# Kernel optimization log

Hardware: AMD Instinct MI355X
Metric: run time of the kernel (lower is better)

Reference implementation:

```python
import jax, jax.numpy as jnp
import numpy as np
from jax import lax

B, S, C = 32, 512, 32          # batch, seq_len (words), char_len
V, E = 101, 64                 # char vocab (printable + pad), emb size
F, K = 128, 3                  # n_filters, kernel_size


def setup_inputs() -> dict:
    key = jax.random.key(0)
    k0, k1, k2, k3 = jax.random.split(key, 4)
    char_ids = jax.random.randint(k0, (B, S, C), 0, V, dtype=jnp.int32)
    emb_table = jax.random.normal(k1, (V, E), dtype=jnp.float32)
    emb_table = emb_table.at[0].set(0.0)  # padding_idx=0
    fan_in = E * K
    conv_w = jax.random.normal(k2, (F, E, K), dtype=jnp.float32) / np.sqrt(fan_in)
    conv_b = jax.random.normal(k3, (F,), dtype=jnp.float32) * 0.01
    return {"char_ids": char_ids, "emb_table": emb_table,
            "conv_w": conv_w, "conv_b": conv_b}


def reference(char_ids, emb_table, conv_w, conv_b):
    b, s, c = char_ids.shape
    e = emb_table.shape[1]
    # embedding lookup: [B, S, C, E]; dropout p=0.0 (eval) -> identity
    char_embs = emb_table[char_ids]
    # FAITHFUL to torch source: .view(-1, E, C) is a raw row-major
    # reinterpretation of the contiguous [B*S, C, E] buffer (not a permute).
    x = char_embs.reshape(b * s, e, c)  # [B*S, E, C] by memory layout
    # Conv1d over the last axis, valid padding
    y = lax.conv_general_dilated(
        x, conv_w, window_strides=(1,), padding="VALID",
        dimension_numbers=("NCH", "OIH", "NCH"))  # [B*S, F, C-K+1]
    y = y + conv_b[None, :, None]
    # max-pool over time, then back to [B, S, F]
    return y.max(axis=2).reshape(b, s, -1)
```

## Files before the change

### kernel.cpp

```cpp
#include <hip/hip_runtime.h>
#include <cstdint>


typedef __bf16 bf16x8 __attribute__((ext_vector_type(8)));
typedef float  f32x16 __attribute__((ext_vector_type(16)));

#define GW   4
#define NGRP 4
#define NW   16
#define ROWS 34
#define RST  72

__global__ __launch_bounds__(256)
void prep_pack_w(const float* __restrict__ w, __bf16* __restrict__ pw) {
  int i = blockIdx.x * 256 + threadIdx.x;
  int j    = i & 7;
  int lane = (i >> 3) & 63;
  int ks   = (i >> 9) & 3;
  int t    = i >> 11;
  int kk   = t % 3;
  int nt   = t / 3;
  int f = nt * 32 + (lane & 31);
  int e = ks * 16 + (lane >> 5) * 8 + j;
  pw[i] = (__bf16)w[f * 192 + e * 3 + kk];
}

__global__ __launch_bounds__(256, 2)
void charcnn_mfma(const int* __restrict__ cid, const float* __restrict__ emb,
                  const float* __restrict__ bias, const __bf16* __restrict__ pw,
                  float* __restrict__ out) {
  __shared__ __align__(16) __bf16 xT[8][ROWS * RST];

  const int tid  = threadIdx.x;
  const int lane = tid & 63;
  const int wv   = tid >> 6;
  const int np   = wv & 1;
  const int ws   = wv >> 1;

  bf16x8 bfrag[2][12];
  const bf16x8* pwv = (const bf16x8*)pw;
#pragma unroll
  for (int nt = 0; nt < 2; ++nt)
#pragma unroll
    for (int q = 0; q < 12; ++q)
      bfrag[nt][q] = pwv[((np * 2 + nt) * 12 + q) * 64 + lane];

  const float vb0 = bias[(np * 2 + 0) * 32 + (lane & 31)];
  const float vb1 = bias[(np * 2 + 1) * 32 + (lane & 31)];

  const int a  = tid >> 3;
  const int p  = tid & 7;
  const int d0 = p * 4;
  const int bw = blockIdx.x * NW;

  int chw[NW];
#pragma unroll
  for (int w = 0; w < NW; ++w) chw[w] = cid[(bw + w) * 32 + a];

  float4 slo[GW], shi[GW];

  auto stage_load = [&](int g) {
#pragma unroll
    for (int i = 0; i < GW; ++i) {
      const float4* er = (const float4*)(emb + chw[g * GW + i] * 64);
      slo[i] = er[p];
      shi[i] = er[p + 8];
    }
  };

  auto stage_write = [&](int g) {
    const int w0 = g * GW;
#pragma unroll
    for (int i = 0; i < GW; ++i) {
      uint32_t* dst = (uint32_t*)(&xT[(w0 + i) & 7][0]);
      float lv[4] = {slo[i].x, slo[i].y, slo[i].z, slo[i].w};
      float hv[4] = {shi[i].x, shi[i].y, shi[i].z, shi[i].w};
#pragma unroll
      for (int i2 = 0; i2 < 4; ++i2) {
        uint32_t u = ((uint32_t)__builtin_bit_cast(uint16_t, (__bf16)hv[i2]) << 16)
                   |  (uint32_t)__builtin_bit_cast(uint16_t, (__bf16)lv[i2]);
        dst[(d0 + i2) * 36 + a] = u;
      }
    }
  };

  auto finish = [&](const f32x16& acc, float vbv, int fcol, int w) {
    float m01 = fmaxf(acc[0],  acc[1]);
    float m23 = fmaxf(acc[2],  acc[3]);
    float m45 = fmaxf(acc[4],  acc[5]);
    float m67 = fmaxf(acc[6],  acc[7]);
    float m89 = fmaxf(acc[8],  acc[9]);
    float mab = fmaxf(acc[10], acc[11]);
    float mcd = fmaxf(acc[12], acc[13]);
    float q0 = fmaxf(m01, m23);
    float q1 = fmaxf(m45, m67);
    float q2 = fmaxf(m89, mab);
    float m0 = fmaxf(fmaxf(q0, q1), fmaxf(q2, mcd));
    float m1 = fmaxf(acc[14], acc[15]);
    float mm = (lane < 32) ? fmaxf(m0, m1) : m0;
    float other = __shfl_xor(mm, 32, 64);
    float fullmax = fmaxf(mm, other) + vbv;
    if (lane < 32) out[(bw + w) * 128 + fcol + lane] = fullmax;
  };

  auto compute_word = [&](int w) {
    const __bf16* xb = &xT[w & 7][0] + (lane & 31) * RST + (lane >> 5) * 8;
    f32x16 acc0, acc1;
#pragma unroll
    for (int r = 0; r < 16; ++r) { acc0[r] = 0.0f; acc1[r] = 0.0f; }

#pragma unroll
    for (int kk = 0; kk < 3; ++kk) {
#pragma unroll
      for (int ks = 0; ks < 4; ++ks) {
        bf16x8 av = *(const bf16x8*)(xb + kk * RST + ks * 16);
        acc0 = __builtin_amdgcn_mfma_f32_32x32x16_bf16(av, bfrag[0][kk * 4 + ks],
                                                       acc0, 0, 0, 0);
        acc1 = __builtin_amdgcn_mfma_f32_32x32x16_bf16(av, bfrag[1][kk * 4 + ks],
                                                       acc1, 0, 0, 0);
      }
    }
    finish(acc0, vb0, np * 64,      w);
    finish(acc1, vb1, np * 64 + 32, w);
  };

  stage_load(0);
  stage_write(0);
  __syncthreads();

#pragma unroll
  for (int g = 0; g < NGRP; ++g) {
    if (g + 1 < NGRP) stage_load(g + 1);
    compute_word(g * GW + ws);
    compute_word(g * GW + ws + 2);
    if (g + 1 < NGRP) stage_write(g + 1);
    if (g + 1 < NGRP) __syncthreads();
  }
}

extern "C" void kernel_launch(void* const* d_in, const int* in_sizes, int n_in,
                              void* d_out, int out_size, void* d_ws, size_t ws_size,
                              hipStream_t stream) {
  const int*   cid = (const int*)d_in[0];
  const float* emb = (const float*)d_in[1];
  const float* cw  = (const float*)d_in[2];
  const float* cb  = (const float*)d_in[3];
  float* outp = (float*)d_out;
  __bf16* pw = (__bf16*)d_ws;

  hipLaunchKernelGGL(prep_pack_w, dim3(96), dim3(256), 0, stream, cw, pw);
  hipLaunchKernelGGL(charcnn_mfma, dim3(1024), dim3(256), 0, stream,
                     cid, emb, cb, (const __bf16*)pw, outp);
}
```

Baseline: 35.10 us.

## Double-buffer embedding prefetch two groups ahead and raise MFMA wave priority

Halves the staging group size to two words and keeps two register buffers of gathered embedding rows. Loads now run two groups ahead, and each group's LDS write happens before the barrier, so the gather latency can hide behind more compute. The plain sync is replaced by an LDS-only waitcnt plus s_barrier, and the MFMA loop is wrapped in s_setprio to favour matrix work. In exchange there are more barriers per block (eight instead of three) and higher register pressure from the doubled staging buffers.

```diff
diff --git a/kernel.cpp b/kernel.cpp
--- a/kernel.cpp
+++ b/kernel.cpp
@@ -5,8 +5,8 @@
 typedef __bf16 bf16x8 __attribute__((ext_vector_type(8)));
 typedef float  f32x16 __attribute__((ext_vector_type(16)));
 
-#define GW   4
-#define NGRP 4
+#define GW   2
+#define NGRP 8
 #define NW   16
 #define ROWS 34
 #define RST  72
@@ -57,24 +57,24 @@
 #pragma unroll
   for (int w = 0; w < NW; ++w) chw[w] = cid[(bw + w) * 32 + a];
 
-  float4 slo[GW], shi[GW];
+  float4 slo[2][GW], shi[2][GW];
 
-  auto stage_load = [&](int g) {
+  auto stage_load = [&](int g, int s) {
 #pragma unroll
     for (int i = 0; i < GW; ++i) {
       const float4* er = (const float4*)(emb + chw[g * GW + i] * 64);
-      slo[i] = er[p];
-      shi[i] = er[p + 8];
+      slo[s][i] = er[p];
+      shi[s][i] = er[p + 8];
     }
   };
 
-  auto stage_write = [&](int g) {
+  auto stage_write = [&](int g, int s) {
     const int w0 = g * GW;
 #pragma unroll
     for (int i = 0; i < GW; ++i) {
       uint32_t* dst = (uint32_t*)(&xT[(w0 + i) & 7][0]);
-      float lv[4] = {slo[i].x, slo[i].y, slo[i].z, slo[i].w};
-      float hv[4] = {shi[i].x, shi[i].y, shi[i].z, shi[i].w};
+      float lv[4] = {slo[s][i].x, slo[s][i].y, slo[s][i].z, slo[s][i].w};
+      float hv[4] = {shi[s][i].x, shi[s][i].y, shi[s][i].z, shi[s][i].w};
 #pragma unroll
       for (int i2 = 0; i2 < 4; ++i2) {
         uint32_t u = ((uint32_t)__builtin_bit_cast(uint16_t, (__bf16)hv[i2]) << 16)
@@ -109,6 +109,7 @@
 #pragma unroll
     for (int r = 0; r < 16; ++r) { acc0[r] = 0.0f; acc1[r] = 0.0f; }
 
+    __builtin_amdgcn_s_setprio(1);
 #pragma unroll
     for (int kk = 0; kk < 3; ++kk) {
 #pragma unroll
@@ -120,21 +121,24 @@
                                                        acc1, 0, 0, 0);
       }
     }
+    __builtin_amdgcn_s_setprio(0);
     finish(acc0, vb0, np * 64,      w);
     finish(acc1, vb1, np * 64 + 32, w);
   };
 
-  stage_load(0);
-  stage_write(0);
-  __syncthreads();
+  stage_load(0, 0);
+  stage_write(0, 0);
+  stage_load(1, 1);
+  asm volatile("s_waitcnt lgkmcnt(0)" ::: "memory");
+  __builtin_amdgcn_s_barrier();
 
 #pragma unroll
   for (int g = 0; g < NGRP; ++g) {
-    if (g + 1 < NGRP) stage_load(g + 1);
+    if (g + 2 < NGRP) stage_load(g + 2, g & 1);
+    if (g + 1 < NGRP) stage_write(g + 1, (g + 1) & 1);
+    asm volatile("s_waitcnt lgkmcnt(0)" ::: "memory");
+    __builtin_amdgcn_s_barrier();
     compute_word(g * GW + ws);
-    compute_word(g * GW + ws + 2);
-    if (g + 1 < NGRP) stage_write(g + 1);
-    if (g + 1 < NGRP) __syncthreads();
   }
 }
 
```

New measurement: 35.12 us. About the same (+0.1%).

## Assign each wave one filter tile across four words, double words per block

Applied to the files above, without the earlier changes.

Each wave now owns one 32-filter tile and runs four independent MFMA chains over the four words of a group. Before, a wave handled two filter tiles for two words. Each block processes 32 words instead of 16, so the grid is half as large and the weight fragments held in registers are reused across more words. The change also wraps the MFMA loop in s_setprio, swaps __syncthreads for a manual lgkmcnt wait plus barrier, and drops the outer loop unroll. The risks are fewer blocks for latency hiding, four live accumulators raising register pressure, and a barrier on the final iteration that was not there before.

```diff
diff --git a/kernel.cpp b/kernel.cpp
--- a/kernel.cpp
+++ b/kernel.cpp
@@ -6,8 +6,8 @@
 typedef float  f32x16 __attribute__((ext_vector_type(16)));
 
 #define GW   4
-#define NGRP 4
-#define NW   16
+#define NGRP 8
+#define NW   32
 #define ROWS 34
 #define RST  72
 
@@ -34,19 +34,14 @@
   const int tid  = threadIdx.x;
   const int lane = tid & 63;
   const int wv   = tid >> 6;
-  const int np   = wv & 1;
-  const int ws   = wv >> 1;
 
-  bf16x8 bfrag[2][12];
+  bf16x8 bfrag[12];
   const bf16x8* pwv = (const bf16x8*)pw;
 #pragma unroll
-  for (int nt = 0; nt < 2; ++nt)
-#pragma unroll
-    for (int q = 0; q < 12; ++q)
-      bfrag[nt][q] = pwv[((np * 2 + nt) * 12 + q) * 64 + lane];
+  for (int q = 0; q < 12; ++q)
+    bfrag[q] = pwv[(wv * 12 + q) * 64 + lane];
 
-  const float vb0 = bias[(np * 2 + 0) * 32 + (lane & 31)];
-  const float vb1 = bias[(np * 2 + 1) * 32 + (lane & 31)];
+  const float vb = bias[wv * 32 + (lane & 31)];
 
   const int a  = tid >> 3;
   const int p  = tid & 7;
@@ -84,7 +79,7 @@
     }
   };
 
-  auto finish = [&](const f32x16& acc, float vbv, int fcol, int w) {
+  auto finish = [&](const f32x16& acc, int w) {
     float m01 = fmaxf(acc[0],  acc[1]);
     float m23 = fmaxf(acc[2],  acc[3]);
     float m45 = fmaxf(acc[4],  acc[5]);
@@ -99,42 +94,57 @@
     float m1 = fmaxf(acc[14], acc[15]);
     float mm = (lane < 32) ? fmaxf(m0, m1) : m0;
     float other = __shfl_xor(mm, 32, 64);
-    float fullmax = fmaxf(mm, other) + vbv;
-    if (lane < 32) out[(bw + w) * 128 + fcol + lane] = fullmax;
+    float fullmax = fmaxf(mm, other) + vb;
+    if (lane < 32) out[(bw + w) * 128 + wv * 32 + lane] = fullmax;
   };
 
-  auto compute_word = [&](int w) {
-    const __bf16* xb = &xT[w & 7][0] + (lane & 31) * RST + (lane >> 5) * 8;
-    f32x16 acc0, acc1;
+  auto compute_group = [&](int g) {
+    const int w0 = g * GW;
+    const __bf16* xb0 = &xT[(w0 + 0) & 7][0] + (lane & 31) * RST + (lane >> 5) * 8;
+    const __bf16* xb1 = &xT[(w0 + 1) & 7][0] + (lane & 31) * RST + (lane >> 5) * 8;
+    const __bf16* xb2 = &xT[(w0 + 2) & 7][0] + (lane & 31) * RST + (lane >> 5) * 8;
+    const __bf16* xb3 = &xT[(w0 + 3) & 7][0] + (lane & 31) * RST + (lane >> 5) * 8;
+    f32x16 acc0, acc1, acc2, acc3;
 #pragma unroll
-    for (int r = 0; r < 16; ++r) { acc0[r] = 0.0f; acc1[r] = 0.0f; }
+    for (int r = 0; r < 16; ++r) {
+      acc0[r] = 0.0f; acc1[r] = 0.0f; acc2[r] = 0.0f; acc3[r] = 0.0f;
+    }
 
+    __builtin_amdgcn_s_setprio(1);
 #pragma unroll
     for (int kk = 0; kk < 3; ++kk) {
 #pragma unroll
       for (int ks = 0; ks < 4; ++ks) {
-        bf16x8 av = *(const bf16x8*)(xb + kk * RST + ks * 16);
-        acc0 = __builtin_amdgcn_mfma_f32_32x32x16_bf16(av, bfrag[0][kk * 4 + ks],
-                                                       acc0, 0, 0, 0);
-        acc1 = __builtin_amdgcn_mfma_f32_32x32x16_bf16(av, bfrag[1][kk * 4 + ks],
-                                                       acc1, 0, 0, 0);
+        const int off = kk * RST + ks * 16;
+        bf16x8 bq = bfrag[kk * 4 + ks];
+        bf16x8 a0 = *(const bf16x8*)(xb0 + off);
+        bf16x8 a1 = *(const bf16x8*)(xb1 + off);
+        bf16x8 a2 = *(const bf16x8*)(xb2 + off);
+        bf16x8 a3 = *(const bf16x8*)(xb3 + off);
+        acc0 = __builtin_amdgcn_mfma_f32_32x32x16_bf16(a0, bq, acc0, 0, 0, 0);
+        acc1 = __builtin_amdgcn_mfma_f32_32x32x16_bf16(a1, bq, acc1, 0, 0, 0);
+        acc2 = __builtin_amdgcn_mfma_f32_32x32x16_bf16(a2, bq, acc2, 0, 0, 0);
+        acc3 = __builtin_amdgcn_mfma_f32_32x32x16_bf16(a3, bq, acc3, 0, 0, 0);
       }
     }
-    finish(acc0, vb0, np * 64,      w);
-    finish(acc1, vb1, np * 64 + 32, w);
+    __builtin_amdgcn_s_setprio(0);
+    finish(acc0, w0 + 0);
+    finish(acc1, w0 + 1);
+    finish(acc2, w0 + 2);
+    finish(acc3, w0 + 3);
   };
 
   stage_load(0);
   stage_write(0);
-  __syncthreads();
+  asm volatile("s_waitcnt lgkmcnt(0)" ::: "memory");
+  __builtin_amdgcn_s_barrier();
 
-#pragma unroll
   for (int g = 0; g < NGRP; ++g) {
     if (g + 1 < NGRP) stage_load(g + 1);
-    compute_word(g * GW + ws);
-    compute_word(g * GW + ws + 2);
+    compute_group(g);
     if (g + 1 < NGRP) stage_write(g + 1);
-    if (g + 1 < NGRP) __syncthreads();
+    asm volatile("s_waitcnt lgkmcnt(0)" ::: "memory");
+    __builtin_amdgcn_s_barrier();
   }
 }
 
@@ -149,6 +159,6 @@
   __bf16* pw = (__bf16*)d_ws;
 
   hipLaunchKernelGGL(prep_pack_w, dim3(96), dim3(256), 0, stream, cw, pw);
-  hipLaunchKernelGGL(charcnn_mfma, dim3(1024), dim3(256), 0, stream,
+  hipLaunchKernelGGL(charcnn_mfma, dim3(512), dim3(256), 0, stream,
                      cid, emb, cb, (const __bf16*)pw, outp);
 }
```

New measurement: 39.81 us. 1.13x slower.

## Pre-pack bf16 embedding table and stage words per wave without block barriers

Applied to the files above, without the earlier changes.

The prep kernel now also converts the embedding table into packed bf16 pairs, so the main kernel gathers ready-made bf16 rows instead of converting fp32 on the fly. Each wave stages its own words into a private double-buffered LDS region, with character ids shuffled across lanes. This removes the block-wide __syncthreads between groups. The cost is that the two waves sharing a word each stage their own copy, which duplicates gather and LDS writes, and correctness now relies on in-wave LDS ordering.

```diff
diff --git a/kernel.cpp b/kernel.cpp
--- a/kernel.cpp
+++ b/kernel.cpp
@@ -5,31 +5,39 @@
 typedef __bf16 bf16x8 __attribute__((ext_vector_type(8)));
 typedef float  f32x16 __attribute__((ext_vector_type(16)));
 
-#define GW   4
-#define NGRP 4
 #define NW   16
+#define WPW  8
 #define ROWS 34
 #define RST  72
 
 __global__ __launch_bounds__(256)
-void prep_pack_w(const float* __restrict__ w, __bf16* __restrict__ pw) {
+void prep_pack(const float* __restrict__ w, const float* __restrict__ emb,
+               __bf16* __restrict__ pw, uint32_t* __restrict__ Dt) {
   int i = blockIdx.x * 256 + threadIdx.x;
-  int j    = i & 7;
-  int lane = (i >> 3) & 63;
-  int ks   = (i >> 9) & 3;
-  int t    = i >> 11;
-  int kk   = t % 3;
-  int nt   = t / 3;
-  int f = nt * 32 + (lane & 31);
-  int e = ks * 16 + (lane >> 5) * 8 + j;
-  pw[i] = (__bf16)w[f * 192 + e * 3 + kk];
+  if (i < 24576) {
+    int j    = i & 7;
+    int lane = (i >> 3) & 63;
+    int ks   = (i >> 9) & 3;
+    int t    = i >> 11;
+    int kk   = t % 3;
+    int nt   = t / 3;
+    int f = nt * 32 + (lane & 31);
+    int e = ks * 16 + (lane >> 5) * 8 + j;
+    pw[i] = (__bf16)w[f * 192 + e * 3 + kk];
+  } else if (i < 24576 + 3232) {
+    int i2 = i - 24576;
+    int c = i2 >> 5, r = i2 & 31;
+    uint32_t lo = (uint32_t)__builtin_bit_cast(uint16_t, (__bf16)emb[c * 64 + r]);
+    uint32_t hi = (uint32_t)__builtin_bit_cast(uint16_t, (__bf16)emb[c * 64 + 32 + r]);
+    Dt[i2] = (hi << 16) | lo;
+  }
 }
 
 __global__ __launch_bounds__(256, 2)
-void charcnn_mfma(const int* __restrict__ cid, const float* __restrict__ emb,
+void charcnn_mfma(const int* __restrict__ cid, const uint32_t* __restrict__ Dt,
                   const float* __restrict__ bias, const __bf16* __restrict__ pw,
                   float* __restrict__ out) {
-  __shared__ __align__(16) __bf16 xT[8][ROWS * RST];
+  __shared__ __align__(16) __bf16 xT[4][2][ROWS * RST];
 
   const int tid  = threadIdx.x;
   const int lane = tid & 63;
@@ -48,39 +56,33 @@
   const float vb0 = bias[(np * 2 + 0) * 32 + (lane & 31)];
   const float vb1 = bias[(np * 2 + 1) * 32 + (lane & 31)];
 
-  const int a  = tid >> 3;
-  const int p  = tid & 7;
-  const int d0 = p * 4;
   const int bw = blockIdx.x * NW;
 
-  int chw[NW];
+  int c0[WPW];
 #pragma unroll
-  for (int w = 0; w < NW; ++w) chw[w] = cid[(bw + w) * 32 + a];
+  for (int j = 0; j < WPW; ++j)
+    c0[j] = cid[(bw + ws + 2 * j) * 32 + (lane & 31)];
 
-  float4 slo[GW], shi[GW];
+  const int sa = lane >> 1;
+  const int ss = lane & 1;
 
-  auto stage_load = [&](int g) {
+  uint4 sd[4];
+
+  auto stage_load = [&](int j) {
+    int ch = __shfl(c0[j], lane >> 1);
+    const uint4* row = (const uint4*)(Dt + ch * 32) + ss * 4;
 #pragma unroll
-    for (int i = 0; i < GW; ++i) {
-      const float4* er = (const float4*)(emb + chw[g * GW + i] * 64);
-      slo[i] = er[p];
-      shi[i] = er[p + 8];
-    }
+    for (int q = 0; q < 4; ++q) sd[q] = row[q];
   };
 
-  auto stage_write = [&](int g) {
-    const int w0 = g * GW;
+  auto stage_write = [&](__bf16* buf) {
+    uint32_t* d = (uint32_t*)buf + sa;
 #pragma unroll
-    for (int i = 0; i < GW; ++i) {
-      uint32_t* dst = (uint32_t*)(&xT[(w0 + i) & 7][0]);
-      float lv[4] = {slo[i].x, slo[i].y, slo[i].z, slo[i].w};
-      float hv[4] = {shi[i].x, shi[i].y, shi[i].z, shi[i].w};
-#pragma unroll
-      for (int i2 = 0; i2 < 4; ++i2) {
-        uint32_t u = ((uint32_t)__builtin_bit_cast(uint16_t, (__bf16)hv[i2]) << 16)
-                   |  (uint32_t)__builtin_bit_cast(uint16_t, (__bf16)lv[i2]);
-        dst[(d0 + i2) * 36 + a] = u;
-      }
+    for (int q = 0; q < 4; ++q) {
+      d[(16 * ss + q * 4 + 0) * 36] = sd[q].x;
+      d[(16 * ss + q * 4 + 1) * 36] = sd[q].y;
+      d[(16 * ss + q * 4 + 2) * 36] = sd[q].z;
+      d[(16 * ss + q * 4 + 3) * 36] = sd[q].w;
     }
   };
 
@@ -103,8 +105,8 @@
     if (lane < 32) out[(bw + w) * 128 + fcol + lane] = fullmax;
   };
 
-  auto compute_word = [&](int w) {
-    const __bf16* xb = &xT[w & 7][0] + (lane & 31) * RST + (lane >> 5) * 8;
+  auto compute_word = [&](int w, const __bf16* buf) {
+    const __bf16* xb = buf + (lane & 31) * RST + (lane >> 5) * 8;
     f32x16 acc0, acc1;
 #pragma unroll
     for (int r = 0; r < 16; ++r) { acc0[r] = 0.0f; acc1[r] = 0.0f; }
@@ -125,16 +127,13 @@
   };
 
   stage_load(0);
-  stage_write(0);
-  __syncthreads();
+  stage_write(&xT[wv][0][0]);
 
 #pragma unroll
-  for (int g = 0; g < NGRP; ++g) {
-    if (g + 1 < NGRP) stage_load(g + 1);
-    compute_word(g * GW + ws);
-    compute_word(g * GW + ws + 2);
-    if (g + 1 < NGRP) stage_write(g + 1);
-    if (g + 1 < NGRP) __syncthreads();
+  for (int j = 0; j < WPW; ++j) {
+    if (j + 1 < WPW) stage_load(j + 1);
+    compute_word(ws + 2 * j, &xT[wv][j & 1][0]);
+    if (j + 1 < WPW) stage_write(&xT[wv][(j + 1) & 1][0]);
   }
 }
 
@@ -146,9 +145,10 @@
   const float* cw  = (const float*)d_in[2];
   const float* cb  = (const float*)d_in[3];
   float* outp = (float*)d_out;
-  __bf16* pw = (__bf16*)d_ws;
+  __bf16*   pw = (__bf16*)d_ws;
+  uint32_t* Dt = (uint32_t*)((char*)d_ws + 49152);
 
-  hipLaunchKernelGGL(prep_pack_w, dim3(96), dim3(256), 0, stream, cw, pw);
+  hipLaunchKernelGGL(prep_pack, dim3(109), dim3(256), 0, stream, cw, emb, pw, Dt);
   hipLaunchKernelGGL(charcnn_mfma, dim3(1024), dim3(256), 0, stream,
-                     cid, emb, cb, (const __bf16*)pw, outp);
+                     cid, Dt, cb, pw, outp);
 }
```

Measured after the change: 34.96 us. No clear change (-0.4%).
